# Kernel tuning notes

Measured on AMD Instinct MI355X. Metric: run time of the kernel, lower is better.

Reference implementation:

```python
import jax, jax.numpy as jnp
import numpy as np


def _proj(x_flat, w, b):
    # x_flat: (N, C, L), w: (O, C), b: (O,) -> (N, O, L)  (1x1x1 Conv3d)
    return jnp.einsum('oc,ncl->nol', w, x_flat) + b[None, :, None]


def setup_inputs() -> dict:
    key = jax.random.key(0)
    ks = jax.random.split(key, 9)
    C, Ch = 256, 128
    N, T, H, W = 2, 8, 28, 28
    s_in = 1.0 / np.sqrt(C)
    s_h = 1.0 / np.sqrt(Ch)
    return {
        'x': jax.random.normal(ks[0], (N, C, T, H, W), jnp.float32),
        'g_w': jax.random.normal(ks[1], (Ch, C), jnp.float32) * s_in,
        'g_b': jax.random.normal(ks[2], (Ch,), jnp.float32) * 0.01,
        'theta_w': jax.random.normal(ks[3], (Ch, C), jnp.float32) * s_in,
        'theta_b': jax.random.normal(ks[4], (Ch,), jnp.float32) * 0.01,
        'phi_w': jax.random.normal(ks[5], (Ch, C), jnp.float32) * s_in,
        'phi_b': jax.random.normal(ks[6], (Ch,), jnp.float32) * 0.01,
        'wz_w': jax.random.normal(ks[7], (C, Ch), jnp.float32) * s_h,
        'wz_b': jax.random.normal(ks[8], (C,), jnp.float32) * 0.01,
    }


def reference(x, g_w, g_b, theta_w, theta_b, phi_w, phi_b, wz_w, wz_b):
    N, C, T, H, W = x.shape
    L = T * H * W
    xf = x.reshape(N, C, L)                      # (N, C, L)
    g_x = _proj(xf, g_w, g_b)                    # (N, Ch, L)
    theta_x = _proj(xf, theta_w, theta_b)        # (N, Ch, L)
    phi_x = _proj(xf, phi_w, phi_b)              # (N, Ch, L)
    # f[n, i, j] = theta[n, :, i] . phi[n, :, j]
    f = jnp.einsum('nci,ncj->nij', theta_x, phi_x)  # (N, L, L)
    f = jax.nn.softmax(f, axis=-1)
    # y[n, c, i] = sum_j f[n, i, j] * g[n, c, j]
    y = jnp.einsum('nij,ncj->nci', f, g_x)          # (N, Ch, L)
    z = _proj(y, wz_w, wz_b)                        # (N, C, L)
    return z.reshape(N, C, T, H, W) + x
```

## Files before the change

kernel.cpp:

```cpp
#include <hip/hip_runtime.h>
#include <hip/hip_bf16.h>

constexpr int CIN    = 256;
constexpr int CH     = 128;
constexpr int LSEQ   = 6272;
constexpr int NBATCH = 2;
constexpr int NLCH   = NBATCH * LSEQ * CH;
constexpr float SHIFT = 40.0f;

typedef __attribute__((ext_vector_type(8))) __bf16 bf16x8;
typedef __attribute__((ext_vector_type(4))) float  f32x4;

__device__ __forceinline__ float bf_lo(unsigned u) { return __uint_as_float(u << 16); }
__device__ __forceinline__ float bf_hi(unsigned u) { return __uint_as_float(u & 0xffff0000u); }
__device__ __forceinline__ unsigned short f2bf(float f) {
    __hip_bfloat16 h = __float2bfloat16(f);
    return *reinterpret_cast<unsigned short*>(&h);
}
__device__ __forceinline__ float us2f(unsigned short h) {
    return __uint_as_float((unsigned)h << 16);
}

union BF8 { bf16x8 v; unsigned short u[8]; };

__device__ __forceinline__ void split8(float4 a, float4 b, bf16x8& hi, bf16x8& lo) {
    BF8 H, L;
    float f[8] = { a.x, a.y, a.z, a.w, b.x, b.y, b.z, b.w };
    #pragma unroll
    for (int p = 0; p < 8; ++p) {
        unsigned short h = f2bf(f[p]);
        H.u[p] = h;
        L.u[p] = f2bf(f[p] - us2f(h));
    }
    hi = H.v; lo = L.v;
}

#define GLDS16(g, l) __builtin_amdgcn_global_load_lds(                      \
    (const __attribute__((address_space(1))) void*)(g),                     \
    (__attribute__((address_space(3))) void*)(l), 16, 0, 0)

__global__ __launch_bounds__(256) void proj_kernel(
    const float* __restrict__ x,
    const float* __restrict__ th_w, const float* __restrict__ th_b,
    const float* __restrict__ ph_w, const float* __restrict__ ph_b,
    const float* __restrict__ gw,   const float* __restrict__ gb,
    unsigned short* __restrict__ q, unsigned short* __restrict__ k,
    unsigned short* __restrict__ vt)
{
    constexpr int XS = 264;
    __shared__ unsigned short xhi[64][XS];
    __shared__ unsigned short xlo[64][XS];
    unsigned short (*gst)[137] = (unsigned short (*)[137])&xhi[0][0];

    const int t    = threadIdx.x;
    const int n    = blockIdx.y;
    const int l0   = blockIdx.x * 64;
    const int w    = t >> 6;
    const int lane = t & 63;
    const int lo   = lane & 15;
    const int quad = lane >> 4;

    {
        const int c = t;
        const float4* xr = (const float4*)(x + (size_t)(n * CIN + c) * LSEQ + l0);
        #pragma unroll
        for (int g4 = 0; g4 < 16; ++g4) {
            float4 v = xr[g4];
            float f[4] = { v.x, v.y, v.z, v.w };
            #pragma unroll
            for (int j = 0; j < 4; ++j) {
                unsigned short h = f2bf(f[j]);
                xhi[g4 * 4 + j][c] = h;
                xlo[g4 * 4 + j][c] = f2bf(f[j] - us2f(h));
            }
        }
    }

    const float* wrp[6]; float biasv[6];
    #pragma unroll
    for (int j = 0; j < 6; ++j) {
        int gch = 96 * w + 16 * j + lo;
        if (gch < 128)      { wrp[j] = th_w + (size_t)gch * CIN;         biasv[j] = th_b[gch]; }
        else if (gch < 256) { wrp[j] = ph_w + (size_t)(gch - 128) * CIN; biasv[j] = ph_b[gch - 128]; }
        else                { wrp[j] = gw   + (size_t)(gch - 256) * CIN; biasv[j] = gb[gch - 256]; }
    }

    f32x4 acc[4][6];
    #pragma unroll
    for (int mt = 0; mt < 4; ++mt)
        #pragma unroll
        for (int j = 0; j < 6; ++j) acc[mt][j] = (f32x4){0.f, 0.f, 0.f, 0.f};

    __syncthreads();

    for (int ks = 0; ks < 8; ++ks) {
        const int k0 = ks * 32 + quad * 8;
        bf16x8 ahi[4], alo[4];
        #pragma unroll
        for (int mt = 0; mt < 4; ++mt) {
            ahi[mt] = *(const bf16x8*)&xhi[mt * 16 + lo][k0];
            alo[mt] = *(const bf16x8*)&xlo[mt * 16 + lo][k0];
        }
        #pragma unroll
        for (int j = 0; j < 6; ++j) {
            const float* p = wrp[j] + k0;
            bf16x8 bhi, blo;
            split8(*(const float4*)p, *(const float4*)(p + 4), bhi, blo);
            #pragma unroll
            for (int mt = 0; mt < 4; ++mt) {
                f32x4 a = acc[mt][j];
                a = __builtin_amdgcn_mfma_f32_16x16x32_bf16(ahi[mt], bhi, a, 0, 0, 0);
                a = __builtin_amdgcn_mfma_f32_16x16x32_bf16(alo[mt], bhi, a, 0, 0, 0);
                a = __builtin_amdgcn_mfma_f32_16x16x32_bf16(ahi[mt], blo, a, 0, 0, 0);
                acc[mt][j] = a;
            }
        }
    }

    __syncthreads();

    #pragma unroll
    for (int j = 0; j < 6; ++j) {
        const int base = 96 * w + 16 * j;
        #pragma unroll
        for (int mt = 0; mt < 4; ++mt) {
            #pragma unroll
            for (int r = 0; r < 4; ++r) {
                float val = acc[mt][j][r] + biasv[j];
                const int lrow = mt * 16 + quad * 4 + r;
                if (base < 256) {
                    unsigned short* dst = (base < 128) ? q : k;
                    const int ch = (base < 128) ? base + lo : base - 128 + lo;
                    dst[(size_t)(n * LSEQ + l0 + lrow) * CH + ch] = f2bf(val);
                } else {
                    gst[lrow][base - 256 + lo] = f2bf(val);
                }
            }
        }
    }
    __syncthreads();

    #pragma unroll
    for (int rep = 0; rep < 16; ++rep) {
        const int flat = rep * 256 + t;
        const int ch   = flat >> 5;
        const int lam  = flat & 31;
        unsigned u = (unsigned)gst[2 * lam][ch] | ((unsigned)gst[2 * lam + 1][ch] << 16);
        ((unsigned*)(vt + (size_t)(n * CH + ch) * LSEQ + l0))[lam] = u;
    }
}

__global__ __launch_bounds__(256, 2) void attn_kernel(
    const unsigned short* __restrict__ qb, const unsigned short* __restrict__ kb,
    const unsigned short* __restrict__ vtg,
    float* __restrict__ Op, float* __restrict__ lp,
    unsigned short* __restrict__ yb, int ns)
{
    constexpr int NTJ = LSEQ / 64;
    __shared__ unsigned short ks [2][64][128];
    __shared__ unsigned short vTs[2][128][64];
    __shared__ unsigned short ps [4][32][64];

    const int t    = threadIdx.x;
    const int s    = blockIdx.y;
    const int n    = blockIdx.z;
    const int i0   = blockIdx.x * 128;
    const int w    = t >> 6;
    const int lane = t & 63;
    const int lo   = lane & 15;
    const int quad = lane >> 4;
    const int lom  = (lo & 7) * 4;

    const int jt0 = (s * NTJ) / ns;
    const int jt1 = ((s + 1) * NTJ) / ns;

    const unsigned short* kbase = kb  + (size_t)n * LSEQ * CH;
    const unsigned short* vbase = vtg + (size_t)n * CH * LSEQ;

    bf16x8 qfrag[2][4];
    #pragma unroll
    for (int mt = 0; mt < 2; ++mt) {
        const unsigned short* qrow =
            qb + (size_t)(n * LSEQ + i0 + 32 * w + mt * 16 + lo) * CH;
        #pragma unroll
        for (int kc = 0; kc < 4; ++kc)
            qfrag[mt][kc] = *(const bf16x8*)(qrow + kc * 32 + quad * 8);
    }

    f32x4 o_acc[2][8];
    #pragma unroll
    for (int mt = 0; mt < 2; ++mt)
        #pragma unroll
        for (int nt = 0; nt < 8; ++nt) o_acc[mt][nt] = (f32x4){0.f, 0.f, 0.f, 0.f};
    float l_r[2][4] = {{0.f,0.f,0.f,0.f},{0.f,0.f,0.f,0.f}};

    auto stage = [&](int buf, int jt) {
        const int j0 = jt * 64;
        #pragma unroll
        for (int i = 0; i < 4; ++i) {
            const int c = w * 4 + i;
            {
                const int row = c * 4 + (lane >> 4);
                const int pcol = (lane & 15) * 4;
                const int lcol = pcol ^ ((row & 7) * 4);
                const unsigned short* g = kbase + (size_t)(j0 + row) * CH + lcol * 2;
                GLDS16(g, &ks[buf][0][0] + c * 512);
            }
            {
                const int row = c * 8 + (lane >> 3);
                const int pcol = (lane & 7) * 4;
                const int lcol = pcol ^ ((row & 7) * 4);
                const unsigned short* g = vbase + (size_t)row * LSEQ + j0 + lcol * 2;
                GLDS16(g, &vTs[buf][0][0] + c * 512);
            }
        }
    };

    int buf = 0;
    stage(0, jt0);
    __syncthreads();

    for (int jt = jt0; jt < jt1; ++jt) {
        if (jt + 1 < jt1) stage(buf ^ 1, jt + 1);

        f32x4 sacc[2][4];
        #pragma unroll
        for (int mt = 0; mt < 2; ++mt)
            #pragma unroll
            for (int ct = 0; ct < 4; ++ct) sacc[mt][ct] = (f32x4){0.f,0.f,0.f,0.f};
        #pragma unroll
        for (int ct = 0; ct < 4; ++ct) {
            #pragma unroll
            for (int kc = 0; kc < 4; ++kc) {
                const int pcol = (kc * 16 + quad * 4) ^ lom;
                bf16x8 b = *(const bf16x8*)&ks[buf][ct * 16 + lo][pcol * 2];
                #pragma unroll
                for (int mt = 0; mt < 2; ++mt)
                    sacc[mt][ct] = __builtin_amdgcn_mfma_f32_16x16x32_bf16(
                        qfrag[mt][kc], b, sacc[mt][ct], 0, 0, 0);
            }
        }

        __builtin_amdgcn_wave_barrier();
        #pragma unroll
        for (int mt = 0; mt < 2; ++mt) {
            #pragma unroll
            for (int ct = 0; ct < 4; ++ct) {
                #pragma unroll
                for (int r = 0; r < 4; ++r) {
                    float p = __expf(sacc[mt][ct][r] - SHIFT);
                    l_r[mt][r] += p;
                    const int row = mt * 16 + quad * 4 + r;
                    const int pdw = (ct * 8 + (lo >> 1)) ^ ((row & 7) * 4);
                    ps[w][row][pdw * 2 + (lo & 1)] = f2bf(p);
                }
            }
        }
        __builtin_amdgcn_wave_barrier();
        __builtin_amdgcn_s_waitcnt(0xC07F);

        bf16x8 pfrag[2][2];
        #pragma unroll
        for (int mt = 0; mt < 2; ++mt)
            #pragma unroll
            for (int kc = 0; kc < 2; ++kc) {
                const int pcol = (kc * 16 + quad * 4) ^ lom;
                pfrag[mt][kc] = *(const bf16x8*)&ps[w][mt * 16 + lo][pcol * 2];
            }

        #pragma unroll
        for (int nt = 0; nt < 8; ++nt) {
            #pragma unroll
            for (int kc = 0; kc < 2; ++kc) {
                const int pcol = (kc * 16 + quad * 4) ^ lom;
                bf16x8 b = *(const bf16x8*)&vTs[buf][nt * 16 + lo][pcol * 2];
                #pragma unroll
                for (int mt = 0; mt < 2; ++mt)
                    o_acc[mt][nt] = __builtin_amdgcn_mfma_f32_16x16x32_bf16(
                        pfrag[mt][kc], b, o_acc[mt][nt], 0, 0, 0);
            }
        }

        __syncthreads();
        buf ^= 1;
    }

    #pragma unroll
    for (int mt = 0; mt < 2; ++mt)
        #pragma unroll
        for (int r = 0; r < 4; ++r) {
            #pragma unroll
            for (int off = 1; off < 16; off <<= 1)
                l_r[mt][r] += __shfl_xor(l_r[mt][r], off);
        }

    if (Op != nullptr) {
        #pragma unroll
        for (int mt = 0; mt < 2; ++mt)
            #pragma unroll
            for (int r = 0; r < 4; ++r) {
                const int qi = i0 + 32 * w + mt * 16 + quad * 4 + r;
                float* orow = Op + ((size_t)(n * ns + s) * LSEQ + qi) * CH;
                #pragma unroll
                for (int nt = 0; nt < 8; ++nt)
                    orow[nt * 16 + lo] = o_acc[mt][nt][r];
                if (lo == 0)
                    lp[(size_t)(n * ns + s) * LSEQ + qi] = l_r[mt][r];
            }
    } else {
        #pragma unroll
        for (int mt = 0; mt < 2; ++mt)
            #pragma unroll
            for (int r = 0; r < 4; ++r) {
                const int qi = i0 + 32 * w + mt * 16 + quad * 4 + r;
                const float inv = 1.0f / l_r[mt][r];
                unsigned short* yr = yb + (size_t)(n * LSEQ + qi) * CH;
                #pragma unroll
                for (int nt = 0; nt < 8; ++nt)
                    yr[nt * 16 + lo] = f2bf(o_acc[mt][nt][r] * inv);
            }
    }
}

__global__ __launch_bounds__(256) void combine_kernel(
    const float* __restrict__ Op, const float* __restrict__ lp,
    unsigned short* __restrict__ yb, int ns)
{
    const int idx = blockIdx.x * 256 + threadIdx.x;
    const int n   = idx / (LSEQ * 32);
    const int rem = idx - n * (LSEQ * 32);
    const int l   = rem >> 5;
    const int c4  = (rem & 31) << 2;

    float4 o = make_float4(0.f, 0.f, 0.f, 0.f);
    float ls = 0.f;
    for (int s = 0; s < ns; ++s) {
        const float4 v = *(const float4*)&Op[((size_t)(n * ns + s) * LSEQ + l) * CH + c4];
        o.x += v.x; o.y += v.y; o.z += v.z; o.w += v.w;
        ls += lp[(size_t)(n * ns + s) * LSEQ + l];
    }
    const float inv = 1.0f / ls;
    unsigned r0 = (unsigned)f2bf(o.x * inv) | ((unsigned)f2bf(o.y * inv) << 16);
    unsigned r1 = (unsigned)f2bf(o.z * inv) | ((unsigned)f2bf(o.w * inv) << 16);
    uint2* dst = (uint2*)(yb + (size_t)(n * LSEQ + l) * CH + c4);
    *dst = make_uint2(r0, r1);
}

__global__ __launch_bounds__(256) void zout_kernel(
    const unsigned short* __restrict__ yb,
    const float* __restrict__ wz_w, const float* __restrict__ wz_b,
    const float* __restrict__ x, float* __restrict__ out)
{
    const int t    = threadIdx.x;
    const int n    = blockIdx.y;
    const int l0   = blockIdx.x * 64;
    const int w    = t >> 6;
    const int lane = t & 63;
    const int lo   = lane & 15;
    const int quad = lane >> 4;

    f32x4 acc[4][4];
    #pragma unroll
    for (int mt = 0; mt < 4; ++mt)
        #pragma unroll
        for (int nt = 0; nt < 4; ++nt) acc[mt][nt] = (f32x4){0.f, 0.f, 0.f, 0.f};

    const unsigned short* yrow[4];
    #pragma unroll
    for (int nt = 0; nt < 4; ++nt)
        yrow[nt] = yb + (size_t)(n * LSEQ + l0 + nt * 16 + lo) * CH;

    #pragma unroll
    for (int ks = 0; ks < 4; ++ks) {
        const int k0 = ks * 32 + quad * 8;
        bf16x8 bfr[4];
        #pragma unroll
        for (int nt = 0; nt < 4; ++nt)
            bfr[nt] = *(const bf16x8*)(yrow[nt] + k0);
        #pragma unroll
        for (int mt = 0; mt < 4; ++mt) {
            const float* p = wz_w + (size_t)(64 * w + mt * 16 + lo) * CH + k0;
            bf16x8 ahi, alo;
            split8(*(const float4*)p, *(const float4*)(p + 4), ahi, alo);
            #pragma unroll
            for (int nt = 0; nt < 4; ++nt) {
                f32x4 a = acc[mt][nt];
                a = __builtin_amdgcn_mfma_f32_16x16x32_bf16(ahi, bfr[nt], a, 0, 0, 0);
                a = __builtin_amdgcn_mfma_f32_16x16x32_bf16(alo, bfr[nt], a, 0, 0, 0);
                acc[mt][nt] = a;
            }
        }
    }

    #pragma unroll
    for (int mt = 0; mt < 4; ++mt) {
        #pragma unroll
        for (int r = 0; r < 4; ++r) {
            const int c = 64 * w + mt * 16 + quad * 4 + r;
            const float bias = wz_b[c];
            const size_t base = (size_t)(n * CIN + c) * LSEQ + l0;
            #pragma unroll
            for (int nt = 0; nt < 4; ++nt) {
                const size_t off = base + nt * 16 + lo;
                out[off] = acc[mt][nt][r] + bias + x[off];
            }
        }
    }
}

extern "C" void kernel_launch(void* const* d_in, const int* in_sizes, int n_in,
                              void* d_out, int out_size, void* d_ws, size_t ws_size,
                              hipStream_t stream) {
    const float* x    = (const float*)d_in[0];
    const float* g_w  = (const float*)d_in[1];
    const float* g_b  = (const float*)d_in[2];
    const float* th_w = (const float*)d_in[3];
    const float* th_b = (const float*)d_in[4];
    const float* ph_w = (const float*)d_in[5];
    const float* ph_b = (const float*)d_in[6];
    const float* wz_w = (const float*)d_in[7];
    const float* wz_b = (const float*)d_in[8];
    float* out = (float*)d_out;

    unsigned short* q  = (unsigned short*)d_ws;
    unsigned short* k  = q + NLCH;
    unsigned short* vt = k + NLCH;
    unsigned short* y  = vt + NLCH;

    const size_t base = (size_t)4 * NLCH * 2;
    const size_t per  = (size_t)NLCH * 4 + (size_t)NBATCH * LSEQ * 4;
    int ns = 0;
    if      (ws_size >= base + 4 * per) ns = 4;
    else if (ws_size >= base + 2 * per) ns = 2;
    else if (ws_size >= base + 1 * per) ns = 1;

    float* Op = (ns > 0) ? (float*)(y + NLCH) : nullptr;
    float* lp = (ns > 0) ? Op + (size_t)ns * NLCH : nullptr;

    proj_kernel<<<dim3(LSEQ / 64, NBATCH), 256, 0, stream>>>(
        x, th_w, th_b, ph_w, ph_b, g_w, g_b, q, k, vt);

    if (ns > 0) {
        attn_kernel<<<dim3(LSEQ / 128, ns, NBATCH), 256, 0, stream>>>(
            q, k, vt, Op, lp, y, ns);
        combine_kernel<<<(NBATCH * LSEQ * 32) / 256, 256, 0, stream>>>(Op, lp, y, ns);
    } else {
        attn_kernel<<<dim3(LSEQ / 128, 1, NBATCH), 256, 0, stream>>>(
            q, k, vt, nullptr, nullptr, y, 1);
    }

    zout_kernel<<<dim3(LSEQ / 64, NBATCH), 256, 0, stream>>>(y, wz_w, wz_b, x, out);
}
```

Before: 190.9 us.

## Shrink tiles, raise split-KV count and attention occupancy, fuse combine into zout

Attention key tiles shrink from 64 to 32 columns, which cuts shared memory per block so the launch bound can ask for 4 blocks per CU. The split-KV factor can now reach 8 when the workspace allows. The separate combine kernel is removed: its partial-sum reduction and normalisation move into the z-projection kernel through a shared-memory staging tile. The projection and zout kernels now use 32-row tiles to launch more blocks. Smaller attention tiles halve the MFMA work per barrier and increase the partial-result traffic from the larger split.

```diff
diff --git a/kernel.cpp b/kernel.cpp
--- a/kernel.cpp
+++ b/kernel.cpp
@@ -12,7 +12,6 @@
 typedef __attribute__((ext_vector_type(4))) float  f32x4;
 
 __device__ __forceinline__ float bf_lo(unsigned u) { return __uint_as_float(u << 16); }
-__device__ __forceinline__ float bf_hi(unsigned u) { return __uint_as_float(u & 0xffff0000u); }
 __device__ __forceinline__ unsigned short f2bf(float f) {
     __hip_bfloat16 h = __float2bfloat16(f);
     return *reinterpret_cast<unsigned short*>(&h);
@@ -48,13 +47,13 @@
     unsigned short* __restrict__ vt)
 {
     constexpr int XS = 264;
-    __shared__ unsigned short xhi[64][XS];
-    __shared__ unsigned short xlo[64][XS];
+    __shared__ unsigned short xhi[32][XS];
+    __shared__ unsigned short xlo[32][XS];
     unsigned short (*gst)[137] = (unsigned short (*)[137])&xhi[0][0];
 
     const int t    = threadIdx.x;
     const int n    = blockIdx.y;
-    const int l0   = blockIdx.x * 64;
+    const int l0   = blockIdx.x * 32;
     const int w    = t >> 6;
     const int lane = t & 63;
     const int lo   = lane & 15;
@@ -64,7 +63,7 @@
         const int c = t;
         const float4* xr = (const float4*)(x + (size_t)(n * CIN + c) * LSEQ + l0);
         #pragma unroll
-        for (int g4 = 0; g4 < 16; ++g4) {
+        for (int g4 = 0; g4 < 8; ++g4) {
             float4 v = xr[g4];
             float f[4] = { v.x, v.y, v.z, v.w };
             #pragma unroll
@@ -85,9 +84,9 @@
         else                { wrp[j] = gw   + (size_t)(gch - 256) * CIN; biasv[j] = gb[gch - 256]; }
     }
 
-    f32x4 acc[4][6];
-    #pragma unroll
-    for (int mt = 0; mt < 4; ++mt)
+    f32x4 acc[2][6];
+    #pragma unroll
+    for (int mt = 0; mt < 2; ++mt)
         #pragma unroll
         for (int j = 0; j < 6; ++j) acc[mt][j] = (f32x4){0.f, 0.f, 0.f, 0.f};
 
@@ -95,9 +94,9 @@
 
     for (int ks = 0; ks < 8; ++ks) {
         const int k0 = ks * 32 + quad * 8;
-        bf16x8 ahi[4], alo[4];
-        #pragma unroll
-        for (int mt = 0; mt < 4; ++mt) {
+        bf16x8 ahi[2], alo[2];
+        #pragma unroll
+        for (int mt = 0; mt < 2; ++mt) {
             ahi[mt] = *(const bf16x8*)&xhi[mt * 16 + lo][k0];
             alo[mt] = *(const bf16x8*)&xlo[mt * 16 + lo][k0];
         }
@@ -107,7 +106,7 @@
             bf16x8 bhi, blo;
             split8(*(const float4*)p, *(const float4*)(p + 4), bhi, blo);
             #pragma unroll
-            for (int mt = 0; mt < 4; ++mt) {
+            for (int mt = 0; mt < 2; ++mt) {
                 f32x4 a = acc[mt][j];
                 a = __builtin_amdgcn_mfma_f32_16x16x32_bf16(ahi[mt], bhi, a, 0, 0, 0);
                 a = __builtin_amdgcn_mfma_f32_16x16x32_bf16(alo[mt], bhi, a, 0, 0, 0);
@@ -123,7 +122,7 @@
     for (int j = 0; j < 6; ++j) {
         const int base = 96 * w + 16 * j;
         #pragma unroll
-        for (int mt = 0; mt < 4; ++mt) {
+        for (int mt = 0; mt < 2; ++mt) {
             #pragma unroll
             for (int r = 0; r < 4; ++r) {
                 float val = acc[mt][j][r] + biasv[j];
@@ -141,25 +140,25 @@
     __syncthreads();
 
     #pragma unroll
-    for (int rep = 0; rep < 16; ++rep) {
+    for (int rep = 0; rep < 8; ++rep) {
         const int flat = rep * 256 + t;
-        const int ch   = flat >> 5;
-        const int lam  = flat & 31;
+        const int ch   = flat >> 4;
+        const int lam  = flat & 15;
         unsigned u = (unsigned)gst[2 * lam][ch] | ((unsigned)gst[2 * lam + 1][ch] << 16);
         ((unsigned*)(vt + (size_t)(n * CH + ch) * LSEQ + l0))[lam] = u;
     }
 }
 
-__global__ __launch_bounds__(256, 2) void attn_kernel(
+__global__ __launch_bounds__(256, 4) void attn_kernel(
     const unsigned short* __restrict__ qb, const unsigned short* __restrict__ kb,
     const unsigned short* __restrict__ vtg,
     float* __restrict__ Op, float* __restrict__ lp,
     unsigned short* __restrict__ yb, int ns)
 {
-    constexpr int NTJ = LSEQ / 64;
-    __shared__ unsigned short ks [2][64][128];
-    __shared__ unsigned short vTs[2][128][64];
-    __shared__ unsigned short ps [4][32][64];
+    constexpr int NTJ = LSEQ / 32;
+    __shared__ unsigned short ks [2][32][128];
+    __shared__ unsigned short vTs[2][128][32];
+    __shared__ unsigned short ps [4][32][32];
 
     const int t    = threadIdx.x;
     const int s    = blockIdx.y;
@@ -169,7 +168,8 @@
     const int lane = t & 63;
     const int lo   = lane & 15;
     const int quad = lane >> 4;
-    const int lom  = (lo & 7) * 4;
+    const int lom7 = (lo & 7) * 4;
+    const int lom3 = (lo & 3) * 4;
 
     const int jt0 = (s * NTJ) / ns;
     const int jt1 = ((s + 1) * NTJ) / ns;
@@ -195,23 +195,21 @@
     float l_r[2][4] = {{0.f,0.f,0.f,0.f},{0.f,0.f,0.f,0.f}};
 
     auto stage = [&](int buf, int jt) {
-        const int j0 = jt * 64;
-        #pragma unroll
-        for (int i = 0; i < 4; ++i) {
-            const int c = w * 4 + i;
+        const int j0 = jt * 32;
+        #pragma unroll
+        for (int i = 0; i < 2; ++i) {
+            const int ck = w * 2 + i;
             {
-                const int row = c * 4 + (lane >> 4);
-                const int pcol = (lane & 15) * 4;
-                const int lcol = pcol ^ ((row & 7) * 4);
-                const unsigned short* g = kbase + (size_t)(j0 + row) * CH + lcol * 2;
-                GLDS16(g, &ks[buf][0][0] + c * 512);
+                const int row = ck * 4 + (lane >> 4);
+                const int ldw = ((lane & 15) * 4) ^ ((row & 7) * 4);
+                const unsigned short* g = kbase + (size_t)(j0 + row) * CH + ldw * 2;
+                GLDS16(g, &ks[buf][0][0] + ck * 512);
             }
             {
-                const int row = c * 8 + (lane >> 3);
-                const int pcol = (lane & 7) * 4;
-                const int lcol = pcol ^ ((row & 7) * 4);
-                const unsigned short* g = vbase + (size_t)row * LSEQ + j0 + lcol * 2;
-                GLDS16(g, &vTs[buf][0][0] + c * 512);
+                const int row = ck * 16 + (lane >> 2);
+                const int ldw = ((lane & 3) * 4) ^ ((row & 3) * 4);
+                const unsigned short* g = vbase + (size_t)row * LSEQ + j0 + ldw * 2;
+                GLDS16(g, &vTs[buf][0][0] + ck * 512);
             }
         }
     };
@@ -223,17 +221,17 @@
     for (int jt = jt0; jt < jt1; ++jt) {
         if (jt + 1 < jt1) stage(buf ^ 1, jt + 1);
 
-        f32x4 sacc[2][4];
+        f32x4 sacc[2][2];
         #pragma unroll
         for (int mt = 0; mt < 2; ++mt)
             #pragma unroll
-            for (int ct = 0; ct < 4; ++ct) sacc[mt][ct] = (f32x4){0.f,0.f,0.f,0.f};
-        #pragma unroll
-        for (int ct = 0; ct < 4; ++ct) {
+            for (int ct = 0; ct < 2; ++ct) sacc[mt][ct] = (f32x4){0.f,0.f,0.f,0.f};
+        #pragma unroll
+        for (int ct = 0; ct < 2; ++ct) {
             #pragma unroll
             for (int kc = 0; kc < 4; ++kc) {
-                const int pcol = (kc * 16 + quad * 4) ^ lom;
-                bf16x8 b = *(const bf16x8*)&ks[buf][ct * 16 + lo][pcol * 2];
+                bf16x8 b = *(const bf16x8*)
+                    &ks[buf][ct * 16 + lo][((kc * 16 + quad * 4) ^ lom7) * 2];
                 #pragma unroll
                 for (int mt = 0; mt < 2; ++mt)
                     sacc[mt][ct] = __builtin_amdgcn_mfma_f32_16x16x32_bf16(
@@ -245,13 +243,13 @@
         #pragma unroll
         for (int mt = 0; mt < 2; ++mt) {
             #pragma unroll
-            for (int ct = 0; ct < 4; ++ct) {
+            for (int ct = 0; ct < 2; ++ct) {
                 #pragma unroll
                 for (int r = 0; r < 4; ++r) {
                     float p = __expf(sacc[mt][ct][r] - SHIFT);
                     l_r[mt][r] += p;
                     const int row = mt * 16 + quad * 4 + r;
-                    const int pdw = (ct * 8 + (lo >> 1)) ^ ((row & 7) * 4);
+                    const int pdw = (ct * 8 + (lo >> 1)) ^ ((row & 3) * 4);
                     ps[w][row][pdw * 2 + (lo & 1)] = f2bf(p);
                 }
             }
@@ -259,26 +257,20 @@
         __builtin_amdgcn_wave_barrier();
         __builtin_amdgcn_s_waitcnt(0xC07F);
 
-        bf16x8 pfrag[2][2];
+        bf16x8 pfrag[2];
         #pragma unroll
         for (int mt = 0; mt < 2; ++mt)
-            #pragma unroll
-            for (int kc = 0; kc < 2; ++kc) {
-                const int pcol = (kc * 16 + quad * 4) ^ lom;
-                pfrag[mt][kc] = *(const bf16x8*)&ps[w][mt * 16 + lo][pcol * 2];
-            }
+            pfrag[mt] = *(const bf16x8*)
+                &ps[w][mt * 16 + lo][((quad * 4) ^ lom3) * 2];
 
         #pragma unroll
         for (int nt = 0; nt < 8; ++nt) {
-            #pragma unroll
-            for (int kc = 0; kc < 2; ++kc) {
-                const int pcol = (kc * 16 + quad * 4) ^ lom;
-                bf16x8 b = *(const bf16x8*)&vTs[buf][nt * 16 + lo][pcol * 2];
-                #pragma unroll
-                for (int mt = 0; mt < 2; ++mt)
-                    o_acc[mt][nt] = __builtin_amdgcn_mfma_f32_16x16x32_bf16(
-                        pfrag[mt][kc], b, o_acc[mt][nt], 0, 0, 0);
-            }
+            bf16x8 b = *(const bf16x8*)
+                &vTs[buf][nt * 16 + lo][((quad * 4) ^ lom3) * 2];
+            #pragma unroll
+            for (int mt = 0; mt < 2; ++mt)
+                o_acc[mt][nt] = __builtin_amdgcn_mfma_f32_16x16x32_bf16(
+                    pfrag[mt], b, o_acc[mt][nt], 0, 0, 0);
         }
 
         __syncthreads();
@@ -322,68 +314,79 @@
     }
 }
 
-__global__ __launch_bounds__(256) void combine_kernel(
+__global__ __launch_bounds__(256) void zout_kernel(
     const float* __restrict__ Op, const float* __restrict__ lp,
-    unsigned short* __restrict__ yb, int ns)
-{
-    const int idx = blockIdx.x * 256 + threadIdx.x;
-    const int n   = idx / (LSEQ * 32);
-    const int rem = idx - n * (LSEQ * 32);
-    const int l   = rem >> 5;
-    const int c4  = (rem & 31) << 2;
-
-    float4 o = make_float4(0.f, 0.f, 0.f, 0.f);
-    float ls = 0.f;
-    for (int s = 0; s < ns; ++s) {
-        const float4 v = *(const float4*)&Op[((size_t)(n * ns + s) * LSEQ + l) * CH + c4];
-        o.x += v.x; o.y += v.y; o.z += v.z; o.w += v.w;
-        ls += lp[(size_t)(n * ns + s) * LSEQ + l];
-    }
-    const float inv = 1.0f / ls;
-    unsigned r0 = (unsigned)f2bf(o.x * inv) | ((unsigned)f2bf(o.y * inv) << 16);
-    unsigned r1 = (unsigned)f2bf(o.z * inv) | ((unsigned)f2bf(o.w * inv) << 16);
-    uint2* dst = (uint2*)(yb + (size_t)(n * LSEQ + l) * CH + c4);
-    *dst = make_uint2(r0, r1);
-}
-
-__global__ __launch_bounds__(256) void zout_kernel(
     const unsigned short* __restrict__ yb,
     const float* __restrict__ wz_w, const float* __restrict__ wz_b,
-    const float* __restrict__ x, float* __restrict__ out)
+    const float* __restrict__ x, float* __restrict__ out, int ns)
 {
+    __shared__ unsigned short ysT[32][136];
+    __shared__ float linv[32];
+
     const int t    = threadIdx.x;
     const int n    = blockIdx.y;
-    const int l0   = blockIdx.x * 64;
+    const int l0   = blockIdx.x * 32;
     const int w    = t >> 6;
     const int lane = t & 63;
     const int lo   = lane & 15;
     const int quad = lane >> 4;
 
-    f32x4 acc[4][4];
+    if (ns > 0) {
+        if (t < 32) {
+            float ls = 0.f;
+            for (int s = 0; s < ns; ++s)
+                ls += lp[(size_t)(n * ns + s) * LSEQ + l0 + t];
+            linv[t] = 1.0f / ls;
+        }
+        __syncthreads();
+        #pragma unroll
+        for (int rep = 0; rep < 4; ++rep) {
+            const int flat = rep * 256 + t;
+            const int l  = flat >> 5;
+            const int c4 = (flat & 31) * 4;
+            float4 o = make_float4(0.f, 0.f, 0.f, 0.f);
+            for (int s = 0; s < ns; ++s) {
+                const float4 v = *(const float4*)
+                    &Op[((size_t)(n * ns + s) * LSEQ + l0 + l) * CH + c4];
+                o.x += v.x; o.y += v.y; o.z += v.z; o.w += v.w;
+            }
+            const float iv = linv[l];
+            unsigned r0 = (unsigned)f2bf(o.x * iv) | ((unsigned)f2bf(o.y * iv) << 16);
+            unsigned r1 = (unsigned)f2bf(o.z * iv) | ((unsigned)f2bf(o.w * iv) << 16);
+            *(uint2*)&ysT[l][c4] = make_uint2(r0, r1);
+        }
+    } else {
+        #pragma unroll
+        for (int rep = 0; rep < 4; ++rep) {
+            const int flat = rep * 256 + t;
+            const int l  = flat >> 5;
+            const int cu = flat & 31;
+            unsigned u = ((const unsigned*)(yb + (size_t)(n * LSEQ + l0 + l) * CH))[cu];
+            *(unsigned*)&ysT[l][cu * 2] = u;
+        }
+    }
+    __syncthreads();
+
+    f32x4 acc[4][2];
     #pragma unroll
     for (int mt = 0; mt < 4; ++mt)
         #pragma unroll
-        for (int nt = 0; nt < 4; ++nt) acc[mt][nt] = (f32x4){0.f, 0.f, 0.f, 0.f};
-
-    const unsigned short* yrow[4];
-    #pragma unroll
-    for (int nt = 0; nt < 4; ++nt)
-        yrow[nt] = yb + (size_t)(n * LSEQ + l0 + nt * 16 + lo) * CH;
+        for (int nt = 0; nt < 2; ++nt) acc[mt][nt] = (f32x4){0.f, 0.f, 0.f, 0.f};
 
     #pragma unroll
     for (int ks = 0; ks < 4; ++ks) {
         const int k0 = ks * 32 + quad * 8;
-        bf16x8 bfr[4];
-        #pragma unroll
-        for (int nt = 0; nt < 4; ++nt)
-            bfr[nt] = *(const bf16x8*)(yrow[nt] + k0);
+        bf16x8 bfr[2];
+        #pragma unroll
+        for (int nt = 0; nt < 2; ++nt)
+            bfr[nt] = *(const bf16x8*)&ysT[nt * 16 + lo][k0];
         #pragma unroll
         for (int mt = 0; mt < 4; ++mt) {
             const float* p = wz_w + (size_t)(64 * w + mt * 16 + lo) * CH + k0;
             bf16x8 ahi, alo;
             split8(*(const float4*)p, *(const float4*)(p + 4), ahi, alo);
             #pragma unroll
-            for (int nt = 0; nt < 4; ++nt) {
+            for (int nt = 0; nt < 2; ++nt) {
                 f32x4 a = acc[mt][nt];
                 a = __builtin_amdgcn_mfma_f32_16x16x32_bf16(ahi, bfr[nt], a, 0, 0, 0);
                 a = __builtin_amdgcn_mfma_f32_16x16x32_bf16(alo, bfr[nt], a, 0, 0, 0);
@@ -400,7 +403,7 @@
             const float bias = wz_b[c];
             const size_t base = (size_t)(n * CIN + c) * LSEQ + l0;
             #pragma unroll
-            for (int nt = 0; nt < 4; ++nt) {
+            for (int nt = 0; nt < 2; ++nt) {
                 const size_t off = base + nt * 16 + lo;
                 out[off] = acc[mt][nt][r] + bias + x[off];
             }
@@ -430,24 +433,25 @@
     const size_t base = (size_t)4 * NLCH * 2;
     const size_t per  = (size_t)NLCH * 4 + (size_t)NBATCH * LSEQ * 4;
     int ns = 0;
-    if      (ws_size >= base + 4 * per) ns = 4;
+    if      (ws_size >= base + 8 * per) ns = 8;
+    else if (ws_size >= base + 4 * per) ns = 4;
     else if (ws_size >= base + 2 * per) ns = 2;
     else if (ws_size >= base + 1 * per) ns = 1;
 
     float* Op = (ns > 0) ? (float*)(y + NLCH) : nullptr;
     float* lp = (ns > 0) ? Op + (size_t)ns * NLCH : nullptr;
 
-    proj_kernel<<<dim3(LSEQ / 64, NBATCH), 256, 0, stream>>>(
+    proj_kernel<<<dim3(LSEQ / 32, NBATCH), 256, 0, stream>>>(
         x, th_w, th_b, ph_w, ph_b, g_w, g_b, q, k, vt);
 
     if (ns > 0) {
         attn_kernel<<<dim3(LSEQ / 128, ns, NBATCH), 256, 0, stream>>>(
             q, k, vt, Op, lp, y, ns);
-        combine_kernel<<<(NBATCH * LSEQ * 32) / 256, 256, 0, stream>>>(Op, lp, y, ns);
     } else {
         attn_kernel<<<dim3(LSEQ / 128, 1, NBATCH), 256, 0, stream>>>(
             q, k, vt, nullptr, nullptr, y, 1);
     }
 
-    zout_kernel<<<dim3(LSEQ / 64, NBATCH), 256, 0, stream>>>(y, wz_w, wz_b, x, out);
-}
+    zout_kernel<<<dim3(LSEQ / 32, NBATCH), 256, 0, stream>>>(
+        Op, lp, y, wz_w, wz_b, x, out, ns);
+}
```

After: 261.2 us. +36.8%, slower.
